# Kernel tuning notes

Hardware: AMD Instinct MI355X
Metric: run time of the kernel (lower is better)

Reference implementation:

```python
import jax, jax.numpy as jnp
import numpy as np

N = 16777216  # points per iteration
D = 3         # spatial dimension of the IFS
K = 8         # number of affine transforms


def setup_inputs() -> dict:
    key = jax.random.key(0)
    ks = jax.random.split(key, 6)
    points = jax.random.normal(ks[0], (N, D), dtype=jnp.float32)
    prev_colors = jax.random.uniform(ks[1], (N, 3), dtype=jnp.float32)
    choices = jax.random.randint(ks[2], (N,), 0, K, dtype=jnp.int32)
    matrices = jax.random.normal(ks[3], (K, D, D), dtype=jnp.float32) * 0.5
    biases = jax.random.normal(ks[4], (K, D), dtype=jnp.float32) * 0.1
    colors = jax.random.uniform(ks[5], (K, 3), dtype=jnp.float32)  # already /255-normalized
    return {"points": points, "prev_colors": prev_colors, "choices": choices,
            "matrices": matrices, "biases": biases, "colors": colors}


def reference(points, prev_colors, choices, matrices, biases, colors):
    # Gather the per-point transform (equivalent of self.matrices[choices] etc.)
    sel_m = matrices[choices]          # [N, D, D]
    sel_b = biases[choices]            # [N, D]
    # torch.bmm(points.unsqueeze(1), sel_m).squeeze(1) == points @ sel_m
    # i.e. contract points over the FIRST axis of each D x D matrix.
    tp = jnp.einsum('nd,nde->ne', points, sel_m) + sel_b
    tp = jax.nn.selu(tp)               # activation='selu'
    new_colors = (prev_colors + colors[choices]) * 0.5
    return tp, new_colors
```

## Files before the change

kernel.cpp:

```cpp
#include <hip/hip_runtime.h>
#include <cstdint>


__device__ __forceinline__ float selu_f(float x) {
    const float alpha = 1.6732632423543772f;
    const float scale = 1.0507009873554805f;
    float neg = alpha * (__expf(x) - 1.0f);
    return scale * (x > 0.0f ? x : neg);
}

__global__ __launch_bounds__(256) void ifs_kernel(
    const float* __restrict__ points,
    const float* __restrict__ prev_colors,
    const int*   __restrict__ choices,
    const float* __restrict__ matrices,
    const float* __restrict__ biases,
    const float* __restrict__ colors,
    float* __restrict__ out_tp,
    float* __restrict__ out_col,
    long long n_points)
{
    __shared__ float T[8][17];
    int tid = threadIdx.x;
    if (tid < 8 * 16) {
        int k = tid >> 4, j = tid & 15;
        float v = 0.0f;
        if (j < 9)       v = matrices[k * 9 + j];
        else if (j < 12) v = biases[k * 3 + (j - 9)];
        else if (j < 15) v = colors[k * 3 + (j - 12)];
        T[k][j] = v;
    }
    __syncthreads();

    long long g = (long long)blockIdx.x * blockDim.x + tid;
    long long base = g * 4;
    if (base >= n_points) return;

    if (base + 4 <= n_points) {
        float4 pv[3], cv[3];
        const float4* pp = reinterpret_cast<const float4*>(points + base * 3);
        const float4* pc = reinterpret_cast<const float4*>(prev_colors + base * 3);
        const int4*   cc = reinterpret_cast<const int4*>(choices + base);
        pv[0] = pp[0]; pv[1] = pp[1]; pv[2] = pp[2];
        cv[0] = pc[0]; cv[1] = pc[1]; cv[2] = pc[2];
        int4 ch = cc[0];

        const float* pb = reinterpret_cast<const float*>(pv);
        const float* cb = reinterpret_cast<const float*>(cv);
        const int*   ci = reinterpret_cast<const int*>(&ch);

        float4 ov[3], oc[3];
        float* ob  = reinterpret_cast<float*>(ov);
        float* ocb = reinterpret_cast<float*>(oc);

        #pragma unroll
        for (int j = 0; j < 4; ++j) {
            int k = ci[j] & 7;
            const float* t = T[k];
            float x = pb[3 * j + 0];
            float y = pb[3 * j + 1];
            float z = pb[3 * j + 2];
            float e0 = fmaf(x, t[0], fmaf(y, t[3], fmaf(z, t[6], t[9])));
            float e1 = fmaf(x, t[1], fmaf(y, t[4], fmaf(z, t[7], t[10])));
            float e2 = fmaf(x, t[2], fmaf(y, t[5], fmaf(z, t[8], t[11])));
            ob[3 * j + 0] = selu_f(e0);
            ob[3 * j + 1] = selu_f(e1);
            ob[3 * j + 2] = selu_f(e2);
            ocb[3 * j + 0] = (cb[3 * j + 0] + t[12]) * 0.5f;
            ocb[3 * j + 1] = (cb[3 * j + 1] + t[13]) * 0.5f;
            ocb[3 * j + 2] = (cb[3 * j + 2] + t[14]) * 0.5f;
        }

        float4* ot = reinterpret_cast<float4*>(out_tp + base * 3);
        float4* oo = reinterpret_cast<float4*>(out_col + base * 3);
        ot[0] = ov[0]; ot[1] = ov[1]; ot[2] = ov[2];
        oo[0] = oc[0]; oo[1] = oc[1]; oo[2] = oc[2];
    } else {
        for (long long p = base; p < n_points; ++p) {
            int k = choices[p] & 7;
            const float* t = T[k];
            float x = points[p * 3 + 0];
            float y = points[p * 3 + 1];
            float z = points[p * 3 + 2];
            float e0 = fmaf(x, t[0], fmaf(y, t[3], fmaf(z, t[6], t[9])));
            float e1 = fmaf(x, t[1], fmaf(y, t[4], fmaf(z, t[7], t[10])));
            float e2 = fmaf(x, t[2], fmaf(y, t[5], fmaf(z, t[8], t[11])));
            out_tp[p * 3 + 0] = selu_f(e0);
            out_tp[p * 3 + 1] = selu_f(e1);
            out_tp[p * 3 + 2] = selu_f(e2);
            out_col[p * 3 + 0] = (prev_colors[p * 3 + 0] + t[12]) * 0.5f;
            out_col[p * 3 + 1] = (prev_colors[p * 3 + 1] + t[13]) * 0.5f;
            out_col[p * 3 + 2] = (prev_colors[p * 3 + 2] + t[14]) * 0.5f;
        }
    }
}

extern "C" void kernel_launch(void* const* d_in, const int* in_sizes, int n_in,
                              void* d_out, int out_size, void* d_ws, size_t ws_size,
                              hipStream_t stream) {
    const float* points      = (const float*)d_in[0];
    const float* prev_colors = (const float*)d_in[1];
    const int*   choices     = (const int*)d_in[2];
    const float* matrices    = (const float*)d_in[3];
    const float* biases      = (const float*)d_in[4];
    const float* colors      = (const float*)d_in[5];

    long long n = in_sizes[2];
    float* out_tp  = (float*)d_out;
    float* out_col = out_tp + (size_t)n * 3;

    long long n_threads = (n + 3) / 4;
    int block = 256;
    long long grid = (n_threads + block - 1) / block;
    ifs_kernel<<<(dim3)(unsigned int)grid, block, 0, stream>>>(
        points, prev_colors, choices, matrices, biases, colors,
        out_tp, out_col, n);
}
```

Baseline: 692.1 us.

## Map each thread to one output float4 with phase-based neighbor gathering

The kernel switches from one thread handling 4 points (three float4 loads per stream, strided by 48 bytes) to one thread per output float4. Each thread loads its own float4 plus both neighbors from points and prev_colors, selects by phase mod 3, and computes two points. Loads and stores become unit-stride across lanes, which gives fully coalesced accesses. In exchange each input float4 is read three times (mostly cache hits), every thread does twice the arithmetic needed, and there are three times as many threads. Inputs whose length is not a multiple of 4 fall back to a scalar kernel.

```diff
diff --git a/kernel.cpp b/kernel.cpp
--- a/kernel.cpp
+++ b/kernel.cpp
@@ -9,16 +9,16 @@
     return scale * (x > 0.0f ? x : neg);
 }
 
-__global__ __launch_bounds__(256) void ifs_kernel(
-    const float* __restrict__ points,
-    const float* __restrict__ prev_colors,
+__global__ __launch_bounds__(256) void ifs_phase_kernel(
+    const float4* __restrict__ pts4,
+    const float4* __restrict__ pcol4,
     const int*   __restrict__ choices,
     const float* __restrict__ matrices,
     const float* __restrict__ biases,
     const float* __restrict__ colors,
-    float* __restrict__ out_tp,
-    float* __restrict__ out_col,
-    long long n_points)
+    float4* __restrict__ out_tp4,
+    float4* __restrict__ out_col4,
+    int F)
 {
     __shared__ float T[8][17];
     int tid = threadIdx.x;
@@ -32,67 +32,87 @@
     }
     __syncthreads();
 
-    long long g = (long long)blockIdx.x * blockDim.x + tid;
-    long long base = g * 4;
-    if (base >= n_points) return;
+    int W = blockIdx.x * 256 + tid;
+    if (W >= F) return;
 
-    if (base + 4 <= n_points) {
-        float4 pv[3], cv[3];
-        const float4* pp = reinterpret_cast<const float4*>(points + base * 3);
-        const float4* pc = reinterpret_cast<const float4*>(prev_colors + base * 3);
-        const int4*   cc = reinterpret_cast<const int4*>(choices + base);
-        pv[0] = pp[0]; pv[1] = pp[1]; pv[2] = pp[2];
-        cv[0] = pc[0]; cv[1] = pc[1]; cv[2] = pc[2];
-        int4 ch = cc[0];
+    int t3  = W / 3;
+    int phi = W - 3 * t3;
+    int p   = W + t3;
+    int Wm = (W == 0)     ? 0     : W - 1;
+    int Wp = (W + 1 < F)  ? W + 1 : F - 1;
 
-        const float* pb = reinterpret_cast<const float*>(pv);
-        const float* cb = reinterpret_cast<const float*>(cv);
-        const int*   ci = reinterpret_cast<const int*>(&ch);
+    float4 A  = pts4[Wm],  B  = pts4[W],  C  = pts4[Wp];
+    float4 Ga = pcol4[Wm], Gb = pcol4[W], Gc = pcol4[Wp];
+    int kp = choices[p] & 7;
+    int kq = choices[p + 1] & 7;
 
-        float4 ov[3], oc[3];
-        float* ob  = reinterpret_cast<float*>(ov);
-        float* ocb = reinterpret_cast<float*>(oc);
+    bool e0 = (phi == 0), e1 = (phi == 1);
 
-        #pragma unroll
-        for (int j = 0; j < 4; ++j) {
-            int k = ci[j] & 7;
-            const float* t = T[k];
-            float x = pb[3 * j + 0];
-            float y = pb[3 * j + 1];
-            float z = pb[3 * j + 2];
-            float e0 = fmaf(x, t[0], fmaf(y, t[3], fmaf(z, t[6], t[9])));
-            float e1 = fmaf(x, t[1], fmaf(y, t[4], fmaf(z, t[7], t[10])));
-            float e2 = fmaf(x, t[2], fmaf(y, t[5], fmaf(z, t[8], t[11])));
-            ob[3 * j + 0] = selu_f(e0);
-            ob[3 * j + 1] = selu_f(e1);
-            ob[3 * j + 2] = selu_f(e2);
-            ocb[3 * j + 0] = (cb[3 * j + 0] + t[12]) * 0.5f;
-            ocb[3 * j + 1] = (cb[3 * j + 1] + t[13]) * 0.5f;
-            ocb[3 * j + 2] = (cb[3 * j + 2] + t[14]) * 0.5f;
-        }
+    float px = e0 ? B.x : e1 ? A.w : A.z;
+    float py = e0 ? B.y : e1 ? B.x : A.w;
+    float pz = e0 ? B.z : e1 ? B.y : B.x;
+    float qx = e0 ? B.w : e1 ? B.z : B.y;
+    float qy = e0 ? C.x : e1 ? B.w : B.z;
+    float qz = e0 ? C.y : e1 ? C.x : B.w;
 
-        float4* ot = reinterpret_cast<float4*>(out_tp + base * 3);
-        float4* oo = reinterpret_cast<float4*>(out_col + base * 3);
-        ot[0] = ov[0]; ot[1] = ov[1]; ot[2] = ov[2];
-        oo[0] = oc[0]; oo[1] = oc[1]; oo[2] = oc[2];
-    } else {
-        for (long long p = base; p < n_points; ++p) {
-            int k = choices[p] & 7;
-            const float* t = T[k];
-            float x = points[p * 3 + 0];
-            float y = points[p * 3 + 1];
-            float z = points[p * 3 + 2];
-            float e0 = fmaf(x, t[0], fmaf(y, t[3], fmaf(z, t[6], t[9])));
-            float e1 = fmaf(x, t[1], fmaf(y, t[4], fmaf(z, t[7], t[10])));
-            float e2 = fmaf(x, t[2], fmaf(y, t[5], fmaf(z, t[8], t[11])));
-            out_tp[p * 3 + 0] = selu_f(e0);
-            out_tp[p * 3 + 1] = selu_f(e1);
-            out_tp[p * 3 + 2] = selu_f(e2);
-            out_col[p * 3 + 0] = (prev_colors[p * 3 + 0] + t[12]) * 0.5f;
-            out_col[p * 3 + 1] = (prev_colors[p * 3 + 1] + t[13]) * 0.5f;
-            out_col[p * 3 + 2] = (prev_colors[p * 3 + 2] + t[14]) * 0.5f;
-        }
-    }
+    float gpx = e0 ? Gb.x : e1 ? Ga.w : Ga.z;
+    float gpy = e0 ? Gb.y : e1 ? Gb.x : Ga.w;
+    float gpz = e0 ? Gb.z : e1 ? Gb.y : Gb.x;
+    float gqx = e0 ? Gb.w : e1 ? Gb.z : Gb.y;
+    float gqy = e0 ? Gc.x : e1 ? Gb.w : Gb.z;
+    float gqz = e0 ? Gc.y : e1 ? Gc.x : Gb.w;
+
+    const float* tp_ = T[kp];
+    const float* tq_ = T[kq];
+
+    float sp0 = selu_f(fmaf(px, tp_[0], fmaf(py, tp_[3], fmaf(pz, tp_[6], tp_[9]))));
+    float sp1 = selu_f(fmaf(px, tp_[1], fmaf(py, tp_[4], fmaf(pz, tp_[7], tp_[10]))));
+    float sp2 = selu_f(fmaf(px, tp_[2], fmaf(py, tp_[5], fmaf(pz, tp_[8], tp_[11]))));
+    float sq0 = selu_f(fmaf(qx, tq_[0], fmaf(qy, tq_[3], fmaf(qz, tq_[6], tq_[9]))));
+    float sq1 = selu_f(fmaf(qx, tq_[1], fmaf(qy, tq_[4], fmaf(qz, tq_[7], tq_[10]))));
+    float sq2 = selu_f(fmaf(qx, tq_[2], fmaf(qy, tq_[5], fmaf(qz, tq_[8], tq_[11]))));
+
+    float cp0 = (gpx + tp_[12]) * 0.5f;
+    float cp1 = (gpy + tp_[13]) * 0.5f;
+    float cp2 = (gpz + tp_[14]) * 0.5f;
+    float cq0 = (gqx + tq_[12]) * 0.5f;
+    float cq1 = (gqy + tq_[13]) * 0.5f;
+    float cq2 = (gqz + tq_[14]) * 0.5f;
+
+    float4 o, oc;
+    o.x  = e0 ? sp0 : e1 ? sp1 : sp2;
+    o.y  = e0 ? sp1 : e1 ? sp2 : sq0;
+    o.z  = e0 ? sp2 : e1 ? sq0 : sq1;
+    o.w  = e0 ? sq0 : e1 ? sq1 : sq2;
+    oc.x = e0 ? cp0 : e1 ? cp1 : cp2;
+    oc.y = e0 ? cp1 : e1 ? cp2 : cq0;
+    oc.z = e0 ? cp2 : e1 ? cq0 : cq1;
+    oc.w = e0 ? cq0 : e1 ? cq1 : cq2;
+
+    out_tp4[W]  = o;
+    out_col4[W] = oc;
+}
+
+__global__ __launch_bounds__(256) void ifs_scalar_kernel(
+    const float* __restrict__ points, const float* __restrict__ prev_colors,
+    const int* __restrict__ choices, const float* __restrict__ matrices,
+    const float* __restrict__ biases, const float* __restrict__ colors,
+    float* __restrict__ out_tp, float* __restrict__ out_col, long long n_points)
+{
+    long long p = (long long)blockIdx.x * blockDim.x + threadIdx.x;
+    if (p >= n_points) return;
+    int k = choices[p] & 7;
+    const float* M = matrices + k * 9;
+    float x = points[p * 3 + 0], y = points[p * 3 + 1], z = points[p * 3 + 2];
+    float e0 = fmaf(x, M[0], fmaf(y, M[3], fmaf(z, M[6], biases[k * 3 + 0])));
+    float e1 = fmaf(x, M[1], fmaf(y, M[4], fmaf(z, M[7], biases[k * 3 + 1])));
+    float e2 = fmaf(x, M[2], fmaf(y, M[5], fmaf(z, M[8], biases[k * 3 + 2])));
+    out_tp[p * 3 + 0] = selu_f(e0);
+    out_tp[p * 3 + 1] = selu_f(e1);
+    out_tp[p * 3 + 2] = selu_f(e2);
+    out_col[p * 3 + 0] = (prev_colors[p * 3 + 0] + colors[k * 3 + 0]) * 0.5f;
+    out_col[p * 3 + 1] = (prev_colors[p * 3 + 1] + colors[k * 3 + 1]) * 0.5f;
+    out_col[p * 3 + 2] = (prev_colors[p * 3 + 2] + colors[k * 3 + 2]) * 0.5f;
 }
 
 extern "C" void kernel_launch(void* const* d_in, const int* in_sizes, int n_in,
@@ -109,10 +129,19 @@
     float* out_tp  = (float*)d_out;
     float* out_col = out_tp + (size_t)n * 3;
 
-    long long n_threads = (n + 3) / 4;
-    int block = 256;
-    long long grid = (n_threads + block - 1) / block;
-    ifs_kernel<<<(dim3)(unsigned int)grid, block, 0, stream>>>(
-        points, prev_colors, choices, matrices, biases, colors,
-        out_tp, out_col, n);
+    if ((n & 3LL) == 0) {
+        int F = (int)(n / 4 * 3);
+        int block = 256;
+        int grid = (F + block - 1) / block;
+        ifs_phase_kernel<<<grid, block, 0, stream>>>(
+            (const float4*)points, (const float4*)prev_colors, choices,
+            matrices, biases, colors,
+            (float4*)out_tp, (float4*)out_col, F);
+    } else {
+        int block = 256;
+        long long grid = (n + block - 1) / block;
+        ifs_scalar_kernel<<<(dim3)(unsigned int)grid, block, 0, stream>>>(
+            points, prev_colors, choices, matrices, biases, colors,
+            out_tp, out_col, n);
+    }
 }
```

Result: faster. 673.4 us (-2.7%).
